# Performance work log

Measured on AMD Instinct MI355X. Metric: run time of the kernel, lower is better.

## Reference

```python
import jax, jax.numpy as jnp
import numpy as np

B, L, D, H = 2, 2048, 1024, 16
HD = D // H
NEG = -1000000000.0


def setup_inputs() -> dict:
    key = jax.random.key(0)
    ks = jax.random.split(key, 11)
    s = 1.0 / np.sqrt(D)
    return {
        "q": jax.random.normal(ks[0], (B, L, D), jnp.float32),
        "k": jax.random.normal(ks[1], (B, L, D), jnp.float32),
        "v": jax.random.normal(ks[2], (B, L, D), jnp.float32),
        "mask": jnp.ones((B, L, L), jnp.int32),
        "Wq": jax.random.normal(ks[3], (D, D), jnp.float32) * s,
        "bq": jnp.zeros((D,), jnp.float32),
        "Wk": jax.random.normal(ks[4], (D, D), jnp.float32) * s,
        "bk": jnp.zeros((D,), jnp.float32),
        "Wv": jax.random.normal(ks[5], (D, D), jnp.float32) * s,
        "bv": jnp.zeros((D,), jnp.float32),
        "Wo": jax.random.normal(ks[6], (D, D), jnp.float32) * s,
        "bo": jnp.zeros((D,), jnp.float32),
    }


def _split(x):
    # [B,L,D] -> [B,H,L,HD]
    return x.reshape(B, L, H, HD).transpose(0, 2, 1, 3)


def reference(q, k, v, mask, Wq, bq, Wk, bk, Wv, bv, Wo, bo):
    Q = _split(q @ Wq.T + bq)
    K = _split(k @ Wk.T + bk)
    V = _split(v @ Wv.T + bv)
    scores = jnp.einsum("bhqd,bhkd->bhqk", Q, K) / jnp.sqrt(jnp.float32(HD))
    m = mask[:, None, :, :]  # [B,1,L,L]
    scores = jnp.where(m == 0, NEG, scores)
    attn = jax.nn.softmax(scores, axis=-1)
    out = jnp.einsum("bhqk,bhkd->bhqd", attn, V)
    out = out.transpose(0, 2, 1, 3).reshape(B, L, D)
    out = out @ Wo.T + bo
    return out, attn
```

## Files before the change

kernel.cpp:

```cpp
#include <hip/hip_runtime.h>
#include <stdint.h>

#define BSZ 2
#define LSEQ 2048
#define DMOD 1024
#define NH 16
#define HDSZ 64

typedef __attribute__((ext_vector_type(8))) short short8;
typedef __attribute__((ext_vector_type(4))) float f32x4;
typedef __attribute__((ext_vector_type(4))) unsigned short u16x4;
typedef __attribute__((ext_vector_type(4))) int i32x4;

#define MFMA16(a, b, c) __builtin_amdgcn_mfma_f32_16x16x32_bf16((a), (b), (c), 0, 0, 0)

__device__ __forceinline__ unsigned short f2bf(float f) {
  union { float f; unsigned u; } x; x.f = f;
  unsigned u = x.u + 0x7fffu + ((x.u >> 16) & 1u);
  return (unsigned short)(u >> 16);
}

__device__ __forceinline__ short8 pack8(f32x4 lo, f32x4 hi) {
  short8 o;
  o[0] = f2bf(lo[0]); o[1] = f2bf(lo[1]); o[2] = f2bf(lo[2]); o[3] = f2bf(lo[3]);
  o[4] = f2bf(hi[0]); o[5] = f2bf(hi[1]); o[6] = f2bf(hi[2]); o[7] = f2bf(hi[3]);
  return o;
}

__global__ __launch_bounds__(256) void mask_check(const int* __restrict__ mask,
                                                  int* __restrict__ flags) {
  const int kt = blockIdx.x, qt = blockIdx.y, b = blockIdx.z;
  const int tid = threadIdx.x;
  const int r = tid >> 1, c = (tid & 1) * 64;
  const int* mr = mask + (size_t)b * LSEQ * LSEQ + (size_t)(qt * 128 + r) * LSEQ + kt * 128 + c;
  int ok = 1;
#pragma unroll
  for (int j = 0; j < 16; j++) {
    i32x4 v = __builtin_nontemporal_load((const i32x4*)(mr + j * 4));
    ok &= (v[0] != 0) & (v[1] != 0) & (v[2] != 0) & (v[3] != 0);
  }
  __shared__ int red[4];
  unsigned long long vote = __ballot(ok);
  if ((tid & 63) == 0) red[tid >> 6] = (vote == ~0ull) ? 1 : 0;
  __syncthreads();
  if (tid == 0) flags[(b * 16 + qt) * 16 + kt] = red[0] & red[1] & red[2] & red[3];
}

template <int AF32, int OUTF32>
__global__ __launch_bounds__(256) void gemm_bt(
    const void* __restrict__ A0, const void* __restrict__ A1, const void* __restrict__ A2,
    const float* __restrict__ W0, const float* __restrict__ W1, const float* __restrict__ W2,
    const float* __restrict__ b0, const float* __restrict__ b1, const float* __restrict__ b2,
    void* __restrict__ C0, void* __restrict__ C1, void* __restrict__ C2,
    float s0, float s1, float s2, int vtz, int M, int N, int K) {
  const int z = blockIdx.z;
  const void* A = (z == 0) ? A0 : ((z == 1) ? A1 : A2);
  const float* W = (z == 0) ? W0 : ((z == 1) ? W1 : W2);
  const float* bias = (z == 0) ? b0 : ((z == 1) ? b1 : b2);
  void* Cout = (z == 0) ? C0 : ((z == 1) ? C1 : C2);
  const float scale = (z == 0) ? s0 : ((z == 1) ? s1 : s2);

  __shared__ unsigned short As[128 * 40];
  __shared__ unsigned short Bs[128 * 40];

  const int tid = threadIdx.x;
  const int lane = tid & 63;
  const int wid = tid >> 6;
  const int bm = blockIdx.x, bn = blockIdx.y;
  const int wm = (wid >> 1) * 64, wn = (wid & 1) * 64;

  f32x4 acc[4][4];
#pragma unroll
  for (int i = 0; i < 4; i++)
#pragma unroll
    for (int j = 0; j < 4; j++) acc[i][j] = (f32x4){0.f, 0.f, 0.f, 0.f};

  const int r0 = tid >> 2;
  const int c0 = (tid & 3) * 8;
  const float* Wg = W + (size_t)(bn * 128 + r0) * K + c0;

  f32x4 vaf[2][2], vbf[2][2];
  short8 vah[2];
  if constexpr (AF32) {
    const float* Ag = (const float*)A + (size_t)(bm * 128 + r0) * K + c0;
#pragma unroll
    for (int j = 0; j < 2; j++) {
      vaf[j][0] = *(const f32x4*)(Ag + (size_t)(j * 64) * K);
      vaf[j][1] = *(const f32x4*)(Ag + (size_t)(j * 64) * K + 4);
    }
  } else {
    const unsigned short* Ag = (const unsigned short*)A + (size_t)(bm * 128 + r0) * K + c0;
#pragma unroll
    for (int j = 0; j < 2; j++) vah[j] = *(const short8*)(Ag + (size_t)(j * 64) * K);
  }
#pragma unroll
  for (int j = 0; j < 2; j++) {
    vbf[j][0] = *(const f32x4*)(Wg + (size_t)(j * 64) * K);
    vbf[j][1] = *(const f32x4*)(Wg + (size_t)(j * 64) * K + 4);
  }

  for (int k0 = 0; k0 < K; k0 += 32) {
#pragma unroll
    for (int j = 0; j < 2; j++) {
      if constexpr (AF32)
        *(short8*)&As[(j * 64 + r0) * 40 + c0] = pack8(vaf[j][0], vaf[j][1]);
      else
        *(short8*)&As[(j * 64 + r0) * 40 + c0] = vah[j];
      *(short8*)&Bs[(j * 64 + r0) * 40 + c0] = pack8(vbf[j][0], vbf[j][1]);
    }
    __syncthreads();
    if (k0 + 32 < K) {
      if constexpr (AF32) {
        const float* Ag = (const float*)A + (size_t)(bm * 128 + r0) * K + c0 + k0 + 32;
#pragma unroll
        for (int j = 0; j < 2; j++) {
          vaf[j][0] = *(const f32x4*)(Ag + (size_t)(j * 64) * K);
          vaf[j][1] = *(const f32x4*)(Ag + (size_t)(j * 64) * K + 4);
        }
      } else {
        const unsigned short* Ag =
            (const unsigned short*)A + (size_t)(bm * 128 + r0) * K + c0 + k0 + 32;
#pragma unroll
        for (int j = 0; j < 2; j++) vah[j] = *(const short8*)(Ag + (size_t)(j * 64) * K);
      }
#pragma unroll
      for (int j = 0; j < 2; j++) {
        vbf[j][0] = *(const f32x4*)(Wg + (size_t)(j * 64) * K + k0 + 32);
        vbf[j][1] = *(const f32x4*)(Wg + (size_t)(j * 64) * K + k0 + 36);
      }
    }
    short8 af[4], bf[4];
#pragma unroll
    for (int i = 0; i < 4; i++)
      af[i] = *(const short8*)&As[(wm + i * 16 + (lane & 15)) * 40 + (lane >> 4) * 8];
#pragma unroll
    for (int i = 0; i < 4; i++)
      bf[i] = *(const short8*)&Bs[(wn + i * 16 + (lane & 15)) * 40 + (lane >> 4) * 8];
#pragma unroll
    for (int i = 0; i < 4; i++)
#pragma unroll
      for (int j = 0; j < 4; j++) acc[i][j] = MFMA16(af[i], bf[j], acc[i][j]);
    __syncthreads();
  }

  const bool vtrans = (z == vtz);
  const int crow = bm * 128 + wm + ((lane >> 4) & 3) * 4;
#pragma unroll
  for (int j = 0; j < 4; j++) {
    const int col = bn * 128 + wn + j * 16 + (lane & 15);
    const float bv = bias[col];
#pragma unroll
    for (int i = 0; i < 4; i++) {
      if (OUTF32) {
#pragma unroll
        for (int r = 0; r < 4; r++) {
          float vvv = (acc[i][j][r] + bv) * scale;
          ((float*)Cout)[(size_t)(crow + i * 16 + r) * N + col] = vvv;
        }
      } else if (vtrans) {
        u16x4 pk;
#pragma unroll
        for (int r = 0; r < 4; r++) pk[r] = f2bf((acc[i][j][r] + bv) * scale);
        const int row = crow + i * 16;
        unsigned short* dst = (unsigned short*)Cout +
                              (size_t)(row >> 11) * DMOD * LSEQ + (size_t)col * LSEQ +
                              (row & (LSEQ - 1));
        *(u16x4*)dst = pk;
      } else {
#pragma unroll
        for (int r = 0; r < 4; r++) {
          float vvv = (acc[i][j][r] + bv) * scale;
          ((unsigned short*)Cout)[(size_t)(crow + i * 16 + r) * N + col] = f2bf(vvv);
        }
      }
    }
  }
}

__global__ __launch_bounds__(256) void attn_kernel(
    const unsigned short* __restrict__ Qp, const unsigned short* __restrict__ Kp,
    const unsigned short* __restrict__ Vt, const int* __restrict__ mask,
    const int* __restrict__ flags, float* __restrict__ attn_out,
    unsigned short* __restrict__ ctx) {
  __shared__ unsigned short Ks[128 * 64];
  __shared__ unsigned short Ps[4][64][68];
  __shared__ float denbuf[2][128];

  const int tid = threadIdx.x, lane = tid & 63, wid = tid >> 6;
  const int kw = wid & 1, qw = wid >> 1;
  const int l15 = lane & 15, lg = lane >> 4;

  const int wgid = blockIdx.x + gridDim.x * blockIdx.y;
  const int jj = wgid >> 3;
  const int bh = (wgid & 7) * 4 + (jj >> 4);
  const int qt = jj & 15;
  const int q0 = qt * 128;
  const int b = bh >> 4, h = bh & 15;

  const unsigned short* Qh = Qp + (size_t)b * LSEQ * DMOD + h * HDSZ;
  const unsigned short* Kh = Kp + (size_t)b * LSEQ * DMOD + h * HDSZ;
  const unsigned short* Vh = Vt + (size_t)b * DMOD * LSEQ + (size_t)h * HDSZ * LSEQ;
  const int* mb = mask + (size_t)b * LSEQ * LSEQ;
  const int* frow = flags + (b * 16 + qt) * 16;
  float* ah = attn_out + (size_t)bh * LSEQ * LSEQ;

  const int wq0 = q0 + qw * 64;
  const int wk0 = kw * 64;

  short8 qf[4][2];
#pragma unroll
  for (int fq = 0; fq < 4; fq++)
#pragma unroll
    for (int ks = 0; ks < 2; ks++)
      qf[fq][ks] = *(const short8*)(Qh + (size_t)(wq0 + fq * 16 + l15) * DMOD +
                                    ks * 32 + lg * 8);

  const int sr = tid >> 1;
  const unsigned short* Kst = Kh + (size_t)sr * DMOD + (tid & 1) * 32;
  const int swz_w = (sr & 7) << 4;

  float den[4] = {0.f, 0.f, 0.f, 0.f};
  short8 ka[4];
#pragma unroll
  for (int j = 0; j < 4; j++) ka[j] = *(const short8*)(Kst + j * 8);

  for (int kt = 0; kt < LSEQ / 128; ++kt) {
    __syncthreads();
#pragma unroll
    for (int j = 0; j < 4; j++)
      *(short8*)&Ks[sr * 64 + (((((tid & 1) * 64) + j * 16) ^ swz_w) >> 1)] = ka[j];
    __syncthreads();
    if (kt + 1 < LSEQ / 128) {
#pragma unroll
      for (int j = 0; j < 4; j++)
        ka[j] = *(const short8*)(Kst + (size_t)(kt + 1) * 128 * DMOD + j * 8);
    }
    const bool fast = frow[kt] != 0;
    if (fast) {
#pragma unroll
      for (int fn = 0; fn < 4; fn++) {
        const int krow = wk0 + fn * 16 + l15;
        const int rb = krow * 64, rx = (krow & 7) << 4;
        short8 kf0 = *(const short8*)&Ks[rb + (((lg * 16) ^ rx) >> 1)];
        short8 kf1 = *(const short8*)&Ks[rb + (((64 + lg * 16) ^ rx) >> 1)];
#pragma unroll
        for (int fq = 0; fq < 4; fq++) {
          f32x4 s = (f32x4){0.f, 0.f, 0.f, 0.f};
          s = MFMA16(kf0, qf[fq][0], s);
          s = MFMA16(kf1, qf[fq][1], s);
          den[fq] += __expf(s[0]) + __expf(s[1]) + __expf(s[2]) + __expf(s[3]);
        }
      }
    } else {
      const int k0 = kt * 128;
#pragma unroll
      for (int fn = 0; fn < 4; fn++) {
        const int krow = wk0 + fn * 16 + l15;
        const int rb = krow * 64, rx = (krow & 7) << 4;
        short8 kf0 = *(const short8*)&Ks[rb + (((lg * 16) ^ rx) >> 1)];
        short8 kf1 = *(const short8*)&Ks[rb + (((64 + lg * 16) ^ rx) >> 1)];
#pragma unroll
        for (int fq = 0; fq < 4; fq++) {
          const int qrow = wq0 + fq * 16 + l15;
          f32x4 s = (f32x4){0.f, 0.f, 0.f, 0.f};
          s = MFMA16(kf0, qf[fq][0], s);
          s = MFMA16(kf1, qf[fq][1], s);
          i32x4 m4 = *(const i32x4*)(mb + (size_t)qrow * LSEQ + k0 + wk0 + fn * 16 + lg * 4);
          den[fq] += (m4[0] != 0) ? __expf(s[0]) : 0.f;
          den[fq] += (m4[1] != 0) ? __expf(s[1]) : 0.f;
          den[fq] += (m4[2] != 0) ? __expf(s[2]) : 0.f;
          den[fq] += (m4[3] != 0) ? __expf(s[3]) : 0.f;
        }
      }
    }
  }
#pragma unroll
  for (int fq = 0; fq < 4; fq++) {
    den[fq] += __shfl_xor(den[fq], 16);
    den[fq] += __shfl_xor(den[fq], 32);
  }
  if (lg == 0) {
#pragma unroll
    for (int fq = 0; fq < 4; fq++) denbuf[kw][qw * 64 + fq * 16 + l15] = den[fq];
  }
  __syncthreads();
  float inv[4];
#pragma unroll
  for (int fq = 0; fq < 4; fq++) {
    const int ql = qw * 64 + fq * 16 + l15;
    inv[fq] = 1.0f / (denbuf[0][ql] + denbuf[1][ql]);
  }

  f32x4 oacc[4][4];
#pragma unroll
  for (int fq = 0; fq < 4; fq++)
#pragma unroll
    for (int fd = 0; fd < 4; fd++) oacc[fq][fd] = (f32x4){0.f, 0.f, 0.f, 0.f};

#pragma unroll
  for (int j = 0; j < 4; j++) ka[j] = *(const short8*)(Kst + j * 8);

  const unsigned short* Vbase = Vh + (size_t)l15 * LSEQ + wk0 + lg * 8;

  for (int kt = 0; kt < LSEQ / 128; ++kt) {
    const int k0 = kt * 128;
    __syncthreads();
#pragma unroll
    for (int j = 0; j < 4; j++)
      *(short8*)&Ks[sr * 64 + (((((tid & 1) * 64) + j * 16) ^ swz_w) >> 1)] = ka[j];
    __syncthreads();
    short8 vf[4][2];
#pragma unroll
    for (int fd = 0; fd < 4; fd++)
#pragma unroll
      for (int ks = 0; ks < 2; ks++)
        vf[fd][ks] = *(const short8*)(Vbase + (size_t)(fd * 16) * LSEQ + k0 + ks * 32);
    if (kt + 1 < LSEQ / 128) {
#pragma unroll
      for (int j = 0; j < 4; j++)
        ka[j] = *(const short8*)(Kst + (size_t)(kt + 1) * 128 * DMOD + j * 8);
    }

    const bool fast = frow[kt] != 0;
    if (fast) {
#pragma unroll
      for (int fn = 0; fn < 4; fn++) {
        const int krow = wk0 + fn * 16 + l15;
        const int rb = krow * 64, rx = (krow & 7) << 4;
        short8 kf0 = *(const short8*)&Ks[rb + (((lg * 16) ^ rx) >> 1)];
        short8 kf1 = *(const short8*)&Ks[rb + (((64 + lg * 16) ^ rx) >> 1)];
#pragma unroll
        for (int fq = 0; fq < 4; fq++) {
          const int qrow = wq0 + fq * 16 + l15;
          f32x4 s = (f32x4){0.f, 0.f, 0.f, 0.f};
          s = MFMA16(kf0, qf[fq][0], s);
          s = MFMA16(kf1, qf[fq][1], s);
          f32x4 a;
          a[0] = __expf(s[0]) * inv[fq];
          a[1] = __expf(s[1]) * inv[fq];
          a[2] = __expf(s[2]) * inv[fq];
          a[3] = __expf(s[3]) * inv[fq];
          __builtin_nontemporal_store(
              a, (f32x4*)(ah + (size_t)qrow * LSEQ + k0 + wk0 + fn * 16 + lg * 4));
          u16x4 pk;
          pk[0] = f2bf(a[0]); pk[1] = f2bf(a[1]); pk[2] = f2bf(a[2]); pk[3] = f2bf(a[3]);
          *(u16x4*)&Ps[wid][fq * 16 + l15][fn * 16 + lg * 4] = pk;
        }
      }
    } else {
#pragma unroll
      for (int fn = 0; fn < 4; fn++) {
        const int krow = wk0 + fn * 16 + l15;
        const int rb = krow * 64, rx = (krow & 7) << 4;
        short8 kf0 = *(const short8*)&Ks[rb + (((lg * 16) ^ rx) >> 1)];
        short8 kf1 = *(const short8*)&Ks[rb + (((64 + lg * 16) ^ rx) >> 1)];
#pragma unroll
        for (int fq = 0; fq < 4; fq++) {
          const int qrow = wq0 + fq * 16 + l15;
          f32x4 s = (f32x4){0.f, 0.f, 0.f, 0.f};
          s = MFMA16(kf0, qf[fq][0], s);
          s = MFMA16(kf1, qf[fq][1], s);
          i32x4 m4 = *(const i32x4*)(mb + (size_t)qrow * LSEQ + k0 + wk0 + fn * 16 + lg * 4);
          f32x4 a;
          a[0] = (m4[0] != 0) ? __expf(s[0]) * inv[fq] : 0.f;
          a[1] = (m4[1] != 0) ? __expf(s[1]) * inv[fq] : 0.f;
          a[2] = (m4[2] != 0) ? __expf(s[2]) * inv[fq] : 0.f;
          a[3] = (m4[3] != 0) ? __expf(s[3]) * inv[fq] : 0.f;
          __builtin_nontemporal_store(
              a, (f32x4*)(ah + (size_t)qrow * LSEQ + k0 + wk0 + fn * 16 + lg * 4));
          u16x4 pk;
          pk[0] = f2bf(a[0]); pk[1] = f2bf(a[1]); pk[2] = f2bf(a[2]); pk[3] = f2bf(a[3]);
          *(u16x4*)&Ps[wid][fq * 16 + l15][fn * 16 + lg * 4] = pk;
        }
      }
    }
    short8 pa2[4][2];
#pragma unroll
    for (int fq = 0; fq < 4; fq++)
#pragma unroll
      for (int ks = 0; ks < 2; ks++)
        pa2[fq][ks] = *(const short8*)&Ps[wid][fq * 16 + l15][ks * 32 + lg * 8];
#pragma unroll
    for (int fd = 0; fd < 4; fd++) {
#pragma unroll
      for (int fq = 0; fq < 4; fq++) {
        oacc[fq][fd] = MFMA16(pa2[fq][0], vf[fd][0], oacc[fq][fd]);
        oacc[fq][fd] = MFMA16(pa2[fq][1], vf[fd][1], oacc[fq][fd]);
      }
    }
  }

  __syncthreads();
  float* red = (float*)&Ps[qw * 2][0][0];
  if (kw == 1) {
#pragma unroll
    for (int fq = 0; fq < 4; fq++)
#pragma unroll
      for (int fd = 0; fd < 4; fd++)
#pragma unroll
        for (int r = 0; r < 4; r++)
          red[(fq * 16 + lg * 4 + r) * 65 + fd * 16 + l15] = oacc[fq][fd][r];
  }
  __syncthreads();
  if (kw == 0) {
    unsigned short* ch = ctx + (size_t)b * LSEQ * DMOD + h * HDSZ;
#pragma unroll
    for (int fq = 0; fq < 4; fq++)
#pragma unroll
      for (int fd = 0; fd < 4; fd++)
#pragma unroll
        for (int r = 0; r < 4; r++) {
          const int qr = wq0 + fq * 16 + lg * 4 + r;
          const float o = oacc[fq][fd][r] + red[(fq * 16 + lg * 4 + r) * 65 + fd * 16 + l15];
          ch[(size_t)qr * DMOD + fd * 16 + l15] = f2bf(o);
        }
  }
}

extern "C" void kernel_launch(void* const* d_in, const int* in_sizes, int n_in,
                              void* d_out, int out_size, void* d_ws, size_t ws_size,
                              hipStream_t stream) {
  const float* q = (const float*)d_in[0];
  const float* k = (const float*)d_in[1];
  const float* v = (const float*)d_in[2];
  const int* mask = (const int*)d_in[3];
  const float* Wq = (const float*)d_in[4];
  const float* bq = (const float*)d_in[5];
  const float* Wk = (const float*)d_in[6];
  const float* bk = (const float*)d_in[7];
  const float* Wv = (const float*)d_in[8];
  const float* bv = (const float*)d_in[9];
  const float* Wo = (const float*)d_in[10];
  const float* bo = (const float*)d_in[11];

  float* out = (float*)d_out;
  float* attn = out + (size_t)BSZ * LSEQ * DMOD;

  const size_t NQKV = (size_t)BSZ * LSEQ * DMOD;

  int* flags = (int*)out;

  unsigned short* Qp = (unsigned short*)d_ws;
  unsigned short* Kp = Qp + NQKV;
  unsigned short* Vt = Kp + NQKV;
  unsigned short* ctx = Vt + NQKV;

  mask_check<<<dim3(16, 16, BSZ), 256, 0, stream>>>(mask, flags);

  gemm_bt<1, 0><<<dim3(32, 8, 3), 256, 0, stream>>>(
      q, k, v, Wq, Wk, Wv, bq, bk, bv, (void*)Qp, (void*)Kp, (void*)Vt,
      0.125f, 1.0f, 1.0f, 2, BSZ * LSEQ, DMOD, DMOD);

  attn_kernel<<<dim3(LSEQ / 128, BSZ * NH), 256, 0, stream>>>(Qp, Kp, Vt, mask, flags,
                                                              attn, ctx);

  gemm_bt<0, 1><<<dim3(32, 8, 1), 256, 0, stream>>>(
      ctx, ctx, ctx, Wo, Wo, Wo, bo, bo, bo, (void*)out, (void*)out, (void*)out,
      1.0f, 1.0f, 1.0f, -1, BSZ * LSEQ, DMOD, DMOD);
}
```

Baseline: 286.0 us.

## Double-buffer K tiles via direct global-to-LDS loads, use exp2 and packed bf16 convert

Replaces the register-staged K tile copy and its two barriers per iteration with a double-buffered LDS scheme. The next tile is fetched with global_load_lds while the current tile is being computed. Folds log2(e) into the Q projection scale so softmax uses the native exp2 instruction, and swaps the manual bf16 rounding for the packed v_cvt_pk_bf16_f32 instruction. This doubles K shared memory, relies on a raw barrier plus vmcnt wait for correctness, and may change rounding slightly.

```diff
diff --git a/kernel.cpp b/kernel.cpp
--- a/kernel.cpp
+++ b/kernel.cpp
@@ -6,6 +6,7 @@
 #define DMOD 1024
 #define NH 16
 #define HDSZ 64
+#define NT (LSEQ / 128)
 
 typedef __attribute__((ext_vector_type(8))) short short8;
 typedef __attribute__((ext_vector_type(4))) float f32x4;
@@ -13,11 +14,20 @@
 typedef __attribute__((ext_vector_type(4))) int i32x4;
 
 #define MFMA16(a, b, c) __builtin_amdgcn_mfma_f32_16x16x32_bf16((a), (b), (c), 0, 0, 0)
+#define EXP2F(x) __builtin_amdgcn_exp2f(x)
+#define WAIT_VM0() asm volatile("s_waitcnt vmcnt(0)" ::: "memory")
+#define RAW_BARRIER() __builtin_amdgcn_s_barrier()
 
 __device__ __forceinline__ unsigned short f2bf(float f) {
   union { float f; unsigned u; } x; x.f = f;
   unsigned u = x.u + 0x7fffu + ((x.u >> 16) & 1u);
   return (unsigned short)(u >> 16);
+}
+
+__device__ __forceinline__ unsigned cvt_pk_bf16(float lo, float hi) {
+  unsigned r;
+  asm("v_cvt_pk_bf16_f32 %0, %1, %2" : "=v"(r) : "v"(lo), "v"(hi));
+  return r;
 }
 
 __device__ __forceinline__ short8 pack8(f32x4 lo, f32x4 hi) {
@@ -177,12 +187,26 @@
   }
 }
 
+__device__ __forceinline__ void stage_k(const unsigned short* __restrict__ Khead, int k0,
+                                        unsigned short* buf, int tid) {
+  const int w = tid >> 6, lane = tid & 63;
+  const int rl = lane >> 3, j = lane & 7;
+#pragma unroll
+  for (int i = 0; i < 4; i++) {
+    const int r = i * 32 + w * 8 + rl;
+    const unsigned short* src = Khead + (size_t)(k0 + r) * DMOD + ((j ^ (r & 7)) << 3);
+    unsigned short* dst = buf + i * 2048 + w * 512;
+    __builtin_amdgcn_global_load_lds((const __attribute__((address_space(1))) void*)src,
+                                     (__attribute__((address_space(3))) void*)dst, 16, 0, 0);
+  }
+}
+
 __global__ __launch_bounds__(256) void attn_kernel(
     const unsigned short* __restrict__ Qp, const unsigned short* __restrict__ Kp,
     const unsigned short* __restrict__ Vt, const int* __restrict__ mask,
     const int* __restrict__ flags, float* __restrict__ attn_out,
     unsigned short* __restrict__ ctx) {
-  __shared__ unsigned short Ks[128 * 64];
+  __shared__ unsigned short Ks[2][128 * 64];
   __shared__ unsigned short Ps[4][64][68];
   __shared__ float denbuf[2][128];
 
@@ -215,40 +239,28 @@
       qf[fq][ks] = *(const short8*)(Qh + (size_t)(wq0 + fq * 16 + l15) * DMOD +
                                     ks * 32 + lg * 8);
 
-  const int sr = tid >> 1;
-  const unsigned short* Kst = Kh + (size_t)sr * DMOD + (tid & 1) * 32;
-  const int swz_w = (sr & 7) << 4;
-
+  stage_k(Kh, 0, &Ks[0][0], tid);
   float den[4] = {0.f, 0.f, 0.f, 0.f};
-  short8 ka[4];
-#pragma unroll
-  for (int j = 0; j < 4; j++) ka[j] = *(const short8*)(Kst + j * 8);
-
-  for (int kt = 0; kt < LSEQ / 128; ++kt) {
-    __syncthreads();
-#pragma unroll
-    for (int j = 0; j < 4; j++)
-      *(short8*)&Ks[sr * 64 + (((((tid & 1) * 64) + j * 16) ^ swz_w) >> 1)] = ka[j];
-    __syncthreads();
-    if (kt + 1 < LSEQ / 128) {
-#pragma unroll
-      for (int j = 0; j < 4; j++)
-        ka[j] = *(const short8*)(Kst + (size_t)(kt + 1) * 128 * DMOD + j * 8);
-    }
+
+  for (int kt = 0; kt < NT; ++kt) {
+    WAIT_VM0();
+    RAW_BARRIER();
+    if (kt + 1 < NT) stage_k(Kh, (kt + 1) * 128, &Ks[(kt + 1) & 1][0], tid);
+    const unsigned short* ksc = &Ks[kt & 1][0];
     const bool fast = frow[kt] != 0;
     if (fast) {
 #pragma unroll
       for (int fn = 0; fn < 4; fn++) {
         const int krow = wk0 + fn * 16 + l15;
         const int rb = krow * 64, rx = (krow & 7) << 4;
-        short8 kf0 = *(const short8*)&Ks[rb + (((lg * 16) ^ rx) >> 1)];
-        short8 kf1 = *(const short8*)&Ks[rb + (((64 + lg * 16) ^ rx) >> 1)];
+        short8 kf0 = *(const short8*)&ksc[rb + (((lg * 16) ^ rx) >> 1)];
+        short8 kf1 = *(const short8*)&ksc[rb + (((64 + lg * 16) ^ rx) >> 1)];
 #pragma unroll
         for (int fq = 0; fq < 4; fq++) {
           f32x4 s = (f32x4){0.f, 0.f, 0.f, 0.f};
           s = MFMA16(kf0, qf[fq][0], s);
           s = MFMA16(kf1, qf[fq][1], s);
-          den[fq] += __expf(s[0]) + __expf(s[1]) + __expf(s[2]) + __expf(s[3]);
+          den[fq] += EXP2F(s[0]) + EXP2F(s[1]) + EXP2F(s[2]) + EXP2F(s[3]);
         }
       }
     } else {
@@ -257,8 +269,8 @@
       for (int fn = 0; fn < 4; fn++) {
         const int krow = wk0 + fn * 16 + l15;
         const int rb = krow * 64, rx = (krow & 7) << 4;
-        short8 kf0 = *(const short8*)&Ks[rb + (((lg * 16) ^ rx) >> 1)];
-        short8 kf1 = *(const short8*)&Ks[rb + (((64 + lg * 16) ^ rx) >> 1)];
+        short8 kf0 = *(const short8*)&ksc[rb + (((lg * 16) ^ rx) >> 1)];
+        short8 kf1 = *(const short8*)&ksc[rb + (((64 + lg * 16) ^ rx) >> 1)];
 #pragma unroll
         for (int fq = 0; fq < 4; fq++) {
           const int qrow = wq0 + fq * 16 + l15;
@@ -266,10 +278,10 @@
           s = MFMA16(kf0, qf[fq][0], s);
           s = MFMA16(kf1, qf[fq][1], s);
           i32x4 m4 = *(const i32x4*)(mb + (size_t)qrow * LSEQ + k0 + wk0 + fn * 16 + lg * 4);
-          den[fq] += (m4[0] != 0) ? __expf(s[0]) : 0.f;
-          den[fq] += (m4[1] != 0) ? __expf(s[1]) : 0.f;
-          den[fq] += (m4[2] != 0) ? __expf(s[2]) : 0.f;
-          den[fq] += (m4[3] != 0) ? __expf(s[3]) : 0.f;
+          den[fq] += (m4[0] != 0) ? EXP2F(s[0]) : 0.f;
+          den[fq] += (m4[1] != 0) ? EXP2F(s[1]) : 0.f;
+          den[fq] += (m4[2] != 0) ? EXP2F(s[2]) : 0.f;
+          den[fq] += (m4[3] != 0) ? EXP2F(s[3]) : 0.f;
         }
       }
     }
@@ -279,6 +291,7 @@
     den[fq] += __shfl_xor(den[fq], 16);
     den[fq] += __shfl_xor(den[fq], 32);
   }
+  stage_k(Kh, 0, &Ks[0][0], tid);
   if (lg == 0) {
 #pragma unroll
     for (int fq = 0; fq < 4; fq++) denbuf[kw][qw * 64 + fq * 16 + l15] = den[fq];
@@ -297,29 +310,20 @@
 #pragma unroll
     for (int fd = 0; fd < 4; fd++) oacc[fq][fd] = (f32x4){0.f, 0.f, 0.f, 0.f};
 
-#pragma unroll
-  for (int j = 0; j < 4; j++) ka[j] = *(const short8*)(Kst + j * 8);
-
   const unsigned short* Vbase = Vh + (size_t)l15 * LSEQ + wk0 + lg * 8;
 
-  for (int kt = 0; kt < LSEQ / 128; ++kt) {
+  for (int kt = 0; kt < NT; ++kt) {
     const int k0 = kt * 128;
-    __syncthreads();
-#pragma unroll
-    for (int j = 0; j < 4; j++)
-      *(short8*)&Ks[sr * 64 + (((((tid & 1) * 64) + j * 16) ^ swz_w) >> 1)] = ka[j];
-    __syncthreads();
+    WAIT_VM0();
+    RAW_BARRIER();
+    const unsigned short* ksc = &Ks[kt & 1][0];
     short8 vf[4][2];
 #pragma unroll
     for (int fd = 0; fd < 4; fd++)
 #pragma unroll
       for (int ks = 0; ks < 2; ks++)
         vf[fd][ks] = *(const short8*)(Vbase + (size_t)(fd * 16) * LSEQ + k0 + ks * 32);
-    if (kt + 1 < LSEQ / 128) {
-#pragma unroll
-      for (int j = 0; j < 4; j++)
-        ka[j] = *(const short8*)(Kst + (size_t)(kt + 1) * 128 * DMOD + j * 8);
-    }
+    if (kt + 1 < NT) stage_k(Kh, (kt + 1) * 128, &Ks[(kt + 1) & 1][0], tid);
 
     const bool fast = frow[kt] != 0;
     if (fast) {
@@ -327,8 +331,8 @@
       for (int fn = 0; fn < 4; fn++) {
         const int krow = wk0 + fn * 16 + l15;
         const int rb = krow * 64, rx = (krow & 7) << 4;
-        short8 kf0 = *(const short8*)&Ks[rb + (((lg * 16) ^ rx) >> 1)];
-        short8 kf1 = *(const short8*)&Ks[rb + (((64 + lg * 16) ^ rx) >> 1)];
+        short8 kf0 = *(const short8*)&ksc[rb + (((lg * 16) ^ rx) >> 1)];
+        short8 kf1 = *(const short8*)&ksc[rb + (((64 + lg * 16) ^ rx) >> 1)];
 #pragma unroll
         for (int fq = 0; fq < 4; fq++) {
           const int qrow = wq0 + fq * 16 + l15;
@@ -336,15 +340,16 @@
           s = MFMA16(kf0, qf[fq][0], s);
           s = MFMA16(kf1, qf[fq][1], s);
           f32x4 a;
-          a[0] = __expf(s[0]) * inv[fq];
-          a[1] = __expf(s[1]) * inv[fq];
-          a[2] = __expf(s[2]) * inv[fq];
-          a[3] = __expf(s[3]) * inv[fq];
+          a[0] = EXP2F(s[0]) * inv[fq];
+          a[1] = EXP2F(s[1]) * inv[fq];
+          a[2] = EXP2F(s[2]) * inv[fq];
+          a[3] = EXP2F(s[3]) * inv[fq];
           __builtin_nontemporal_store(
               a, (f32x4*)(ah + (size_t)qrow * LSEQ + k0 + wk0 + fn * 16 + lg * 4));
-          u16x4 pk;
-          pk[0] = f2bf(a[0]); pk[1] = f2bf(a[1]); pk[2] = f2bf(a[2]); pk[3] = f2bf(a[3]);
-          *(u16x4*)&Ps[wid][fq * 16 + l15][fn * 16 + lg * 4] = pk;
+          union { u16x4 pk; unsigned u[2]; } P;
+          P.u[0] = cvt_pk_bf16(a[0], a[1]);
+          P.u[1] = cvt_pk_bf16(a[2], a[3]);
+          *(u16x4*)&Ps[wid][fq * 16 + l15][fn * 16 + lg * 4] = P.pk;
         }
       }
     } else {
@@ -352,8 +357,8 @@
       for (int fn = 0; fn < 4; fn++) {
         const int krow = wk0 + fn * 16 + l15;
         const int rb = krow * 64, rx = (krow & 7) << 4;
-        short8 kf0 = *(const short8*)&Ks[rb + (((lg * 16) ^ rx) >> 1)];
-        short8 kf1 = *(const short8*)&Ks[rb + (((64 + lg * 16) ^ rx) >> 1)];
+        short8 kf0 = *(const short8*)&ksc[rb + (((lg * 16) ^ rx) >> 1)];
+        short8 kf1 = *(const short8*)&ksc[rb + (((64 + lg * 16) ^ rx) >> 1)];
 #pragma unroll
         for (int fq = 0; fq < 4; fq++) {
           const int qrow = wq0 + fq * 16 + l15;
@@ -362,15 +367,16 @@
           s = MFMA16(kf1, qf[fq][1], s);
           i32x4 m4 = *(const i32x4*)(mb + (size_t)qrow * LSEQ + k0 + wk0 + fn * 16 + lg * 4);
           f32x4 a;
-          a[0] = (m4[0] != 0) ? __expf(s[0]) * inv[fq] : 0.f;
-          a[1] = (m4[1] != 0) ? __expf(s[1]) * inv[fq] : 0.f;
-          a[2] = (m4[2] != 0) ? __expf(s[2]) * inv[fq] : 0.f;
-          a[3] = (m4[3] != 0) ? __expf(s[3]) * inv[fq] : 0.f;
+          a[0] = (m4[0] != 0) ? EXP2F(s[0]) * inv[fq] : 0.f;
+          a[1] = (m4[1] != 0) ? EXP2F(s[1]) * inv[fq] : 0.f;
+          a[2] = (m4[2] != 0) ? EXP2F(s[2]) * inv[fq] : 0.f;
+          a[3] = (m4[3] != 0) ? EXP2F(s[3]) * inv[fq] : 0.f;
           __builtin_nontemporal_store(
               a, (f32x4*)(ah + (size_t)qrow * LSEQ + k0 + wk0 + fn * 16 + lg * 4));
-          u16x4 pk;
-          pk[0] = f2bf(a[0]); pk[1] = f2bf(a[1]); pk[2] = f2bf(a[2]); pk[3] = f2bf(a[3]);
-          *(u16x4*)&Ps[wid][fq * 16 + l15][fn * 16 + lg * 4] = pk;
+          union { u16x4 pk; unsigned u[2]; } P;
+          P.u[0] = cvt_pk_bf16(a[0], a[1]);
+          P.u[1] = cvt_pk_bf16(a[2], a[3]);
+          *(u16x4*)&Ps[wid][fq * 16 + l15][fn * 16 + lg * 4] = P.pk;
         }
       }
     }
@@ -449,7 +455,7 @@
 
   gemm_bt<1, 0><<<dim3(32, 8, 3), 256, 0, stream>>>(
       q, k, v, Wq, Wk, Wv, bq, bk, bv, (void*)Qp, (void*)Kp, (void*)Vt,
-      0.125f, 1.0f, 1.0f, 2, BSZ * LSEQ, DMOD, DMOD);
+      0.18033688011112042f, 1.0f, 1.0f, 2, BSZ * LSEQ, DMOD, DMOD);
 
   attn_kernel<<<dim3(LSEQ / 128, BSZ * NH), 256, 0, stream>>>(Qp, Kp, Vt, mask, flags,
                                                               attn, ctx);
```

Result: no change. 291.6 us (+2.0%).

## Split softmax denominator pass into separate kernel and use exp2 with packed bf16 convert

Applied to the files above, without the earlier changes.

Moves the first (denominator) pass of the two-pass attention into its own kernel launched over 1024 workgroups with 64 queries each. Each wave there handles 16 query rows across all 128 keys per tile. It writes inverse denominators to a workspace buffer that the PV kernel reads. The intent is more parallelism and occupancy for the denominator pass. Also folds log2(e) into the Q projection scale so the hardware exp2 instruction replaces expf, and uses v_cvt_pk_bf16_f32 for packing P. This adds a kernel launch and extra workspace use, and reads invbuf past the ctx region.

```diff
diff --git a/kernel.cpp b/kernel.cpp
--- a/kernel.cpp
+++ b/kernel.cpp
@@ -6,6 +6,7 @@
 #define DMOD 1024
 #define NH 16
 #define HDSZ 64
+#define NT (LSEQ / 128)
 
 typedef __attribute__((ext_vector_type(8))) short short8;
 typedef __attribute__((ext_vector_type(4))) float f32x4;
@@ -13,11 +14,18 @@
 typedef __attribute__((ext_vector_type(4))) int i32x4;
 
 #define MFMA16(a, b, c) __builtin_amdgcn_mfma_f32_16x16x32_bf16((a), (b), (c), 0, 0, 0)
+#define EXP2F(x) __builtin_amdgcn_exp2f(x)
 
 __device__ __forceinline__ unsigned short f2bf(float f) {
   union { float f; unsigned u; } x; x.f = f;
   unsigned u = x.u + 0x7fffu + ((x.u >> 16) & 1u);
   return (unsigned short)(u >> 16);
+}
+
+__device__ __forceinline__ unsigned cvt_pk_bf16(float lo, float hi) {
+  unsigned r;
+  asm("v_cvt_pk_bf16_f32 %0, %1, %2" : "=v"(r) : "v"(lo), "v"(hi));
+  return r;
 }
 
 __device__ __forceinline__ short8 pack8(f32x4 lo, f32x4 hi) {
@@ -177,14 +185,99 @@
   }
 }
 
-__global__ __launch_bounds__(256) void attn_kernel(
+__global__ __launch_bounds__(256) void den_kernel(
+    const unsigned short* __restrict__ Qp, const unsigned short* __restrict__ Kp,
+    const int* __restrict__ mask, const int* __restrict__ flags,
+    float* __restrict__ invbuf) {
+  __shared__ unsigned short Ks[128 * 64];
+
+  const int tid = threadIdx.x, lane = tid & 63, wid = tid >> 6;
+  const int l15 = lane & 15, lg = lane >> 4;
+
+  const int wgid = blockIdx.x + gridDim.x * blockIdx.y;
+  const int jj = wgid >> 3;
+  const int bh = (wgid & 7) * 4 + (jj >> 5);
+  const int qb = jj & 31;
+  const int q0 = qb * 64;
+  const int b = bh >> 4, h = bh & 15;
+
+  const unsigned short* Qh = Qp + (size_t)b * LSEQ * DMOD + h * HDSZ;
+  const unsigned short* Kh = Kp + (size_t)b * LSEQ * DMOD + h * HDSZ;
+  const int* mb = mask + (size_t)b * LSEQ * LSEQ;
+  const int* frow = flags + (b * 16 + (q0 >> 7)) * 16;
+
+  const int wq0 = q0 + wid * 16;
+  const int qrow = wq0 + l15;
+
+  short8 qf[2];
+#pragma unroll
+  for (int ks = 0; ks < 2; ks++)
+    qf[ks] = *(const short8*)(Qh + (size_t)qrow * DMOD + ks * 32 + lg * 8);
+
+  const int sr = tid >> 1;
+  const unsigned short* Kst = Kh + (size_t)sr * DMOD + (tid & 1) * 32;
+  const int swz_w = (sr & 7) << 4;
+
+  float den = 0.f;
+  short8 ka[4];
+#pragma unroll
+  for (int j = 0; j < 4; j++) ka[j] = *(const short8*)(Kst + j * 8);
+
+  for (int kt = 0; kt < NT; ++kt) {
+    __syncthreads();
+#pragma unroll
+    for (int j = 0; j < 4; j++)
+      *(short8*)&Ks[sr * 64 + (((((tid & 1) * 64) + j * 16) ^ swz_w) >> 1)] = ka[j];
+    __syncthreads();
+    if (kt + 1 < NT) {
+#pragma unroll
+      for (int j = 0; j < 4; j++)
+        ka[j] = *(const short8*)(Kst + (size_t)(kt + 1) * 128 * DMOD + j * 8);
+    }
+    const bool fast = frow[kt] != 0;
+    if (fast) {
+#pragma unroll
+      for (int fn = 0; fn < 8; fn++) {
+        const int krow = fn * 16 + l15;
+        const int rb = krow * 64, rx = (krow & 7) << 4;
+        short8 kf0 = *(const short8*)&Ks[rb + (((lg * 16) ^ rx) >> 1)];
+        short8 kf1 = *(const short8*)&Ks[rb + (((64 + lg * 16) ^ rx) >> 1)];
+        f32x4 s = (f32x4){0.f, 0.f, 0.f, 0.f};
+        s = MFMA16(kf0, qf[0], s);
+        s = MFMA16(kf1, qf[1], s);
+        den += EXP2F(s[0]) + EXP2F(s[1]) + EXP2F(s[2]) + EXP2F(s[3]);
+      }
+    } else {
+      const int k0 = kt * 128;
+#pragma unroll
+      for (int fn = 0; fn < 8; fn++) {
+        const int krow = fn * 16 + l15;
+        const int rb = krow * 64, rx = (krow & 7) << 4;
+        short8 kf0 = *(const short8*)&Ks[rb + (((lg * 16) ^ rx) >> 1)];
+        short8 kf1 = *(const short8*)&Ks[rb + (((64 + lg * 16) ^ rx) >> 1)];
+        f32x4 s = (f32x4){0.f, 0.f, 0.f, 0.f};
+        s = MFMA16(kf0, qf[0], s);
+        s = MFMA16(kf1, qf[1], s);
+        i32x4 m4 = *(const i32x4*)(mb + (size_t)qrow * LSEQ + k0 + fn * 16 + lg * 4);
+        den += (m4[0] != 0) ? EXP2F(s[0]) : 0.f;
+        den += (m4[1] != 0) ? EXP2F(s[1]) : 0.f;
+        den += (m4[2] != 0) ? EXP2F(s[2]) : 0.f;
+        den += (m4[3] != 0) ? EXP2F(s[3]) : 0.f;
+      }
+    }
+  }
+  den += __shfl_xor(den, 16);
+  den += __shfl_xor(den, 32);
+  if (lg == 0) invbuf[(size_t)bh * LSEQ + qrow] = 1.0f / den;
+}
+
+__global__ __launch_bounds__(256) void pv_kernel(
     const unsigned short* __restrict__ Qp, const unsigned short* __restrict__ Kp,
     const unsigned short* __restrict__ Vt, const int* __restrict__ mask,
-    const int* __restrict__ flags, float* __restrict__ attn_out,
-    unsigned short* __restrict__ ctx) {
+    const int* __restrict__ flags, const float* __restrict__ invbuf,
+    float* __restrict__ attn_out, unsigned short* __restrict__ ctx) {
   __shared__ unsigned short Ks[128 * 64];
   __shared__ unsigned short Ps[4][64][68];
-  __shared__ float denbuf[2][128];
 
   const int tid = threadIdx.x, lane = tid & 63, wid = tid >> 6;
   const int kw = wid & 1, qw = wid >> 1;
@@ -214,108 +307,41 @@
     for (int ks = 0; ks < 2; ks++)
       qf[fq][ks] = *(const short8*)(Qh + (size_t)(wq0 + fq * 16 + l15) * DMOD +
                                     ks * 32 + lg * 8);
+  float inv[4];
+#pragma unroll
+  for (int fq = 0; fq < 4; fq++)
+    inv[fq] = invbuf[(size_t)bh * LSEQ + wq0 + fq * 16 + l15];
 
   const int sr = tid >> 1;
   const unsigned short* Kst = Kh + (size_t)sr * DMOD + (tid & 1) * 32;
   const int swz_w = (sr & 7) << 4;
 
-  float den[4] = {0.f, 0.f, 0.f, 0.f};
+  f32x4 oacc[4][4];
+#pragma unroll
+  for (int fq = 0; fq < 4; fq++)
+#pragma unroll
+    for (int fd = 0; fd < 4; fd++) oacc[fq][fd] = (f32x4){0.f, 0.f, 0.f, 0.f};
+
   short8 ka[4];
 #pragma unroll
   for (int j = 0; j < 4; j++) ka[j] = *(const short8*)(Kst + j * 8);
 
-  for (int kt = 0; kt < LSEQ / 128; ++kt) {
+  const unsigned short* Vbase = Vh + (size_t)l15 * LSEQ + wk0 + lg * 8;
+
+  for (int kt = 0; kt < NT; ++kt) {
+    const int k0 = kt * 128;
     __syncthreads();
 #pragma unroll
     for (int j = 0; j < 4; j++)
       *(short8*)&Ks[sr * 64 + (((((tid & 1) * 64) + j * 16) ^ swz_w) >> 1)] = ka[j];
     __syncthreads();
-    if (kt + 1 < LSEQ / 128) {
-#pragma unroll
-      for (int j = 0; j < 4; j++)
-        ka[j] = *(const short8*)(Kst + (size_t)(kt + 1) * 128 * DMOD + j * 8);
-    }
-    const bool fast = frow[kt] != 0;
-    if (fast) {
-#pragma unroll
-      for (int fn = 0; fn < 4; fn++) {
-        const int krow = wk0 + fn * 16 + l15;
-        const int rb = krow * 64, rx = (krow & 7) << 4;
-        short8 kf0 = *(const short8*)&Ks[rb + (((lg * 16) ^ rx) >> 1)];
-        short8 kf1 = *(const short8*)&Ks[rb + (((64 + lg * 16) ^ rx) >> 1)];
-#pragma unroll
-        for (int fq = 0; fq < 4; fq++) {
-          f32x4 s = (f32x4){0.f, 0.f, 0.f, 0.f};
-          s = MFMA16(kf0, qf[fq][0], s);
-          s = MFMA16(kf1, qf[fq][1], s);
-          den[fq] += __expf(s[0]) + __expf(s[1]) + __expf(s[2]) + __expf(s[3]);
-        }
-      }
-    } else {
-      const int k0 = kt * 128;
-#pragma unroll
-      for (int fn = 0; fn < 4; fn++) {
-        const int krow = wk0 + fn * 16 + l15;
-        const int rb = krow * 64, rx = (krow & 7) << 4;
-        short8 kf0 = *(const short8*)&Ks[rb + (((lg * 16) ^ rx) >> 1)];
-        short8 kf1 = *(const short8*)&Ks[rb + (((64 + lg * 16) ^ rx) >> 1)];
-#pragma unroll
-        for (int fq = 0; fq < 4; fq++) {
-          const int qrow = wq0 + fq * 16 + l15;
-          f32x4 s = (f32x4){0.f, 0.f, 0.f, 0.f};
-          s = MFMA16(kf0, qf[fq][0], s);
-          s = MFMA16(kf1, qf[fq][1], s);
-          i32x4 m4 = *(const i32x4*)(mb + (size_t)qrow * LSEQ + k0 + wk0 + fn * 16 + lg * 4);
-          den[fq] += (m4[0] != 0) ? __expf(s[0]) : 0.f;
-          den[fq] += (m4[1] != 0) ? __expf(s[1]) : 0.f;
-          den[fq] += (m4[2] != 0) ? __expf(s[2]) : 0.f;
-          den[fq] += (m4[3] != 0) ? __expf(s[3]) : 0.f;
-        }
-      }
-    }
-  }
-#pragma unroll
-  for (int fq = 0; fq < 4; fq++) {
-    den[fq] += __shfl_xor(den[fq], 16);
-    den[fq] += __shfl_xor(den[fq], 32);
-  }
-  if (lg == 0) {
-#pragma unroll
-    for (int fq = 0; fq < 4; fq++) denbuf[kw][qw * 64 + fq * 16 + l15] = den[fq];
-  }
-  __syncthreads();
-  float inv[4];
-#pragma unroll
-  for (int fq = 0; fq < 4; fq++) {
-    const int ql = qw * 64 + fq * 16 + l15;
-    inv[fq] = 1.0f / (denbuf[0][ql] + denbuf[1][ql]);
-  }
-
-  f32x4 oacc[4][4];
-#pragma unroll
-  for (int fq = 0; fq < 4; fq++)
-#pragma unroll
-    for (int fd = 0; fd < 4; fd++) oacc[fq][fd] = (f32x4){0.f, 0.f, 0.f, 0.f};
-
-#pragma unroll
-  for (int j = 0; j < 4; j++) ka[j] = *(const short8*)(Kst + j * 8);
-
-  const unsigned short* Vbase = Vh + (size_t)l15 * LSEQ + wk0 + lg * 8;
-
-  for (int kt = 0; kt < LSEQ / 128; ++kt) {
-    const int k0 = kt * 128;
-    __syncthreads();
-#pragma unroll
-    for (int j = 0; j < 4; j++)
-      *(short8*)&Ks[sr * 64 + (((((tid & 1) * 64) + j * 16) ^ swz_w) >> 1)] = ka[j];
-    __syncthreads();
     short8 vf[4][2];
 #pragma unroll
     for (int fd = 0; fd < 4; fd++)
 #pragma unroll
       for (int ks = 0; ks < 2; ks++)
         vf[fd][ks] = *(const short8*)(Vbase + (size_t)(fd * 16) * LSEQ + k0 + ks * 32);
-    if (kt + 1 < LSEQ / 128) {
+    if (kt + 1 < NT) {
 #pragma unroll
       for (int j = 0; j < 4; j++)
         ka[j] = *(const short8*)(Kst + (size_t)(kt + 1) * 128 * DMOD + j * 8);
@@ -336,15 +362,16 @@
           s = MFMA16(kf0, qf[fq][0], s);
           s = MFMA16(kf1, qf[fq][1], s);
           f32x4 a;
-          a[0] = __expf(s[0]) * inv[fq];
-          a[1] = __expf(s[1]) * inv[fq];
-          a[2] = __expf(s[2]) * inv[fq];
-          a[3] = __expf(s[3]) * inv[fq];
+          a[0] = EXP2F(s[0]) * inv[fq];
+          a[1] = EXP2F(s[1]) * inv[fq];
+          a[2] = EXP2F(s[2]) * inv[fq];
+          a[3] = EXP2F(s[3]) * inv[fq];
           __builtin_nontemporal_store(
               a, (f32x4*)(ah + (size_t)qrow * LSEQ + k0 + wk0 + fn * 16 + lg * 4));
-          u16x4 pk;
-          pk[0] = f2bf(a[0]); pk[1] = f2bf(a[1]); pk[2] = f2bf(a[2]); pk[3] = f2bf(a[3]);
-          *(u16x4*)&Ps[wid][fq * 16 + l15][fn * 16 + lg * 4] = pk;
+          union { u16x4 pk; unsigned u[2]; } P;
+          P.u[0] = cvt_pk_bf16(a[0], a[1]);
+          P.u[1] = cvt_pk_bf16(a[2], a[3]);
+          *(u16x4*)&Ps[wid][fq * 16 + l15][fn * 16 + lg * 4] = P.pk;
         }
       }
     } else {
@@ -362,15 +389,16 @@
           s = MFMA16(kf1, qf[fq][1], s);
           i32x4 m4 = *(const i32x4*)(mb + (size_t)qrow * LSEQ + k0 + wk0 + fn * 16 + lg * 4);
           f32x4 a;
-          a[0] = (m4[0] != 0) ? __expf(s[0]) * inv[fq] : 0.f;
-          a[1] = (m4[1] != 0) ? __expf(s[1]) * inv[fq] : 0.f;
-          a[2] = (m4[2] != 0) ? __expf(s[2]) * inv[fq] : 0.f;
-          a[3] = (m4[3] != 0) ? __expf(s[3]) * inv[fq] : 0.f;
+          a[0] = (m4[0] != 0) ? EXP2F(s[0]) * inv[fq] : 0.f;
+          a[1] = (m4[1] != 0) ? EXP2F(s[1]) * inv[fq] : 0.f;
+          a[2] = (m4[2] != 0) ? EXP2F(s[2]) * inv[fq] : 0.f;
+          a[3] = (m4[3] != 0) ? EXP2F(s[3]) * inv[fq] : 0.f;
           __builtin_nontemporal_store(
               a, (f32x4*)(ah + (size_t)qrow * LSEQ + k0 + wk0 + fn * 16 + lg * 4));
-          u16x4 pk;
-          pk[0] = f2bf(a[0]); pk[1] = f2bf(a[1]); pk[2] = f2bf(a[2]); pk[3] = f2bf(a[3]);
-          *(u16x4*)&Ps[wid][fq * 16 + l15][fn * 16 + lg * 4] = pk;
+          union { u16x4 pk; unsigned u[2]; } P;
+          P.u[0] = cvt_pk_bf16(a[0], a[1]);
+          P.u[1] = cvt_pk_bf16(a[2], a[3]);
+          *(u16x4*)&Ps[wid][fq * 16 + l15][fn * 16 + lg * 4] = P.pk;
         }
       }
     }
@@ -444,15 +472,17 @@
   unsigned short* Kp = Qp + NQKV;
   unsigned short* Vt = Kp + NQKV;
   unsigned short* ctx = Vt + NQKV;
+  float* invbuf = (float*)(ctx + NQKV);
 
   mask_check<<<dim3(16, 16, BSZ), 256, 0, stream>>>(mask, flags);
 
   gemm_bt<1, 0><<<dim3(32, 8, 3), 256, 0, stream>>>(
       q, k, v, Wq, Wk, Wv, bq, bk, bv, (void*)Qp, (void*)Kp, (void*)Vt,
-      0.125f, 1.0f, 1.0f, 2, BSZ * LSEQ, DMOD, DMOD);
-
-  attn_kernel<<<dim3(LSEQ / 128, BSZ * NH), 256, 0, stream>>>(Qp, Kp, Vt, mask, flags,
-                                                              attn, ctx);
+      0.18033688011112042f, 1.0f, 1.0f, 2, BSZ * LSEQ, DMOD, DMOD);
+
+  den_kernel<<<dim3(32, 32), 256, 0, stream>>>(Qp, Kp, mask, flags, invbuf);
+
+  pv_kernel<<<dim3(16, 32), 256, 0, stream>>>(Qp, Kp, Vt, mask, flags, invbuf, attn, ctx);
 
   gemm_bt<0, 1><<<dim3(32, 8, 1), 256, 0, stream>>>(
       ctx, ctx, ctx, Wo, Wo, Wo, bo, bo, bo, (void*)out, (void*)out, (void*)out,
```

Result: slower. 300.9 us (+5.2%).
